# Optimization experiments

Hardware: AMD Instinct MI355X
Metric: run time of the kernel (lower is better)

The kernel has to match this reference:

```python
import jax, jax.numpy as jnp
import numpy as np

TS = 4  # tile_size


def _disp_upsample_slanted(d, dx, dy, ts):
    """Slanted-plane disparity upsample (PixelShuffle of per-tile-pixel planes).
    d, dx, dy: [B,1,Ht,Wt] -> full-res disparity [B,1,H,W], H=Ht*ts, W=Wt*ts.
    output[y,x] = d[y//ts,x//ts] + (y%ts - c)*dy + (x%ts - c)*dx, c=(ts-1)/2."""
    B, _, Ht, Wt = d.shape
    c = (ts - 1) / 2
    off = jnp.arange(ts, dtype=d.dtype) - jnp.asarray(c, d.dtype)  # [ts]
    d_, dx_, dy_ = d[:, 0], dx[:, 0], dy[:, 0]  # [B,Ht,Wt]
    off_i = off[None, :, None, None, None]  # row offset within tile
    off_j = off[None, None, :, None, None]  # col offset within tile
    disp = d_[:, None, None] + off_i * dy_[:, None, None] + off_j * dx_[:, None, None]
    # [B,ts_i,ts_j,Ht,Wt] -> pixel-shuffle -> [B,1,H,W]
    disp = disp.transpose(0, 3, 1, 4, 2).reshape(B, 1, Ht * ts, Wt * ts)
    return disp


def _l1_cost_chaos(fea_l, fea_r, disp):
    """Per-pixel horizontal warp of fea_r by continuous disparity (linear interp,
    zero outside image), then L1 distance over channels. Returns [B,1,H,W]."""
    B, C, H, W = fea_l.shape
    x = jnp.arange(W, dtype=disp.dtype)
    x_src = x[None, None, None, :] - disp              # [B,1,H,W]
    x0 = jnp.floor(x_src)
    w = (x_src - x0).astype(fea_r.dtype)
    x0i = jnp.clip(x0.astype(jnp.int32), 0, W - 1)
    x1i = jnp.clip(x0i + 1, 0, W - 1)
    f0 = jnp.take_along_axis(fea_r, jnp.broadcast_to(x0i, (B, C, H, W)), axis=3)
    f1 = jnp.take_along_axis(fea_r, jnp.broadcast_to(x1i, (B, C, H, W)), axis=3)
    warped = f0 * (1.0 - w) + f1 * w
    valid = (x_src >= 0) & (x_src <= W - 1)
    warped = jnp.where(valid, warped, jnp.zeros((), fea_r.dtype))
    return jnp.sum(jnp.abs(fea_l - warped), axis=1, keepdims=True)


def _tile_unshuffle(cv, ts):
    """[B,1,H,W] -> [B, ts*ts, H//ts, W//ts]; channel i*ts+j holds cv[i::ts, j::ts]."""
    B, _, H, W = cv.shape
    Ht, Wt = H // ts, W // ts
    return cv.reshape(B, Ht, ts, Wt, ts).transpose(0, 2, 4, 1, 3).reshape(B, ts * ts, Ht, Wt)


def setup_inputs() -> dict:
    key = jax.random.key(0)
    k1, k2, k3, k4, k5 = jax.random.split(key, 5)
    B, C, H, W, ts = 4, 32, 512, 960, TS
    Ht, Wt = H // ts, W // ts
    d = jax.random.uniform(k1, (B, 1, Ht, Wt), jnp.float32) * 48.0
    dx = jax.random.normal(k2, (B, 1, Ht, Wt), jnp.float32) * 0.1
    dy = jax.random.normal(k3, (B, 1, Ht, Wt), jnp.float32) * 0.1
    tile_plane = jnp.concatenate([d, dx, dy], axis=1)  # [B,3,Ht,Wt]
    fea_l = jax.random.normal(k4, (B, C, H, W), jnp.float32)
    fea_r = jax.random.normal(k5, (B, C, H, W), jnp.float32)
    return {"tile_plane": tile_plane, "fea_l": fea_l, "fea_r": fea_r}


def reference(tile_plane, fea_l, fea_r):
    ts = TS
    tile_d = tile_plane[:, 0:1]
    tile_dx = tile_plane[:, 1:2]
    tile_dy = tile_plane[:, 2:3]
    local_cv = []
    for disp_d in (-1, 0, 1):
        disp_full = _disp_upsample_slanted(tile_d + disp_d, tile_dx, tile_dy, ts)
        cv = _l1_cost_chaos(fea_l, fea_r, disp_full)        # [B,1,H,W]
        local_cv.append(_tile_unshuffle(cv, ts))            # [B,ts*ts,Ht,Wt]
    return jnp.concatenate(local_cv, axis=1)                # [B,3*ts*ts,Ht,Wt]
```

## Files before the change

kernel.cpp:

```cpp
#include <hip/hip_runtime.h>
#include <cstdint>

#define AS1 __attribute__((address_space(1)))
#define AS3 __attribute__((address_space(3)))

constexpr int B  = 4;
constexpr int C  = 32;
constexpr int H  = 512;
constexpr int Wd = 960;
constexpr int Ht = H / 4;
constexpr int Wt = Wd / 4;
constexpr int HW = H * Wd;

constexpr int BLKX  = 256;
constexpr int XMARG = 56;
constexpr int SELEM = BLKX + 64;

__global__ __launch_bounds__(256, 4) void tile_warping_kernel(
    const float* __restrict__ tp,
    const float* __restrict__ fl,
    const float* __restrict__ fr,
    float* __restrict__ out)
{
    __shared__ float sm[SELEM * C];

    const int lane = threadIdx.x;
    const int x0 = blockIdx.x * BLKX;
    const int y  = blockIdx.y;
    const int b  = blockIdx.z;
    const int xstart = x0 - XMARG;

    const float* frrow = fr + ((size_t)b * C * H + y) * Wd;
    #pragma unroll
    for (int chunk = 0; chunk < (SELEM * C) / (BLKX * 4); ++chunk) {
        int e   = chunk * (BLKX * 4) + lane * 4;
        int ch  = e / SELEM;
        int off = e - ch * SELEM;
        int gx  = min(max(xstart + off, 0), Wd - 4);
        const float* gp = frrow + (size_t)ch * HW + gx;
        __builtin_amdgcn_global_load_lds((const AS1 float*)gp,
                                         (AS3 float*)(&sm[e]), 16, 0, 0);
    }
    __syncthreads();

    const int x = x0 + lane;
    if (x < Wd) {
        const int ht = y >> 2, ii = y & 3;
        const int wt = x >> 2, jj = x & 3;

        const int tbase = ((b * 3) * Ht + ht) * Wt + wt;
        const float dv  = tp[tbase];
        const float dxv = tp[tbase + Ht * Wt];
        const float dyv = tp[tbase + 2 * Ht * Wt];

        const float oi = (float)ii - 1.5f;
        const float oj = (float)jj - 1.5f;

        int   o0[3];
        float w[3], w1[3];
        bool  val[3];
        #pragma unroll
        for (int k = 0; k < 3; ++k) {
            float disp = ((dv + (float)(k - 1)) + oi * dyv) + oj * dxv;
            float xs = (float)x - disp;
            float ff = floorf(xs);
            w[k]  = xs - ff;
            w1[k] = 1.0f - w[k];
            int c0 = min(max((int)ff, 0), Wd - 1);
            o0[k]  = c0 - xstart;
            val[k] = (xs >= 0.0f) && (xs <= (float)(Wd - 1));
        }

        const float* flp = fl + ((size_t)b * C * H + y) * Wd + x;

        float s0 = 0.f, s1 = 0.f, s2 = 0.f;
        #pragma unroll 4
        for (int c = 0; c < C; ++c) {
            float l = flp[(size_t)c * HW];
            const float* bp = sm + c * SELEM;
            float f00 = bp[o0[0]], f01 = bp[o0[0] + 1];
            float f10 = bp[o0[1]], f11 = bp[o0[1] + 1];
            float f20 = bp[o0[2]], f21 = bp[o0[2] + 1];
            float wv0 = val[0] ? (f00 * w1[0] + f01 * w[0]) : 0.f;
            float wv1 = val[1] ? (f10 * w1[1] + f11 * w[1]) : 0.f;
            float wv2 = val[2] ? (f20 * w1[2] + f21 * w[2]) : 0.f;
            s0 += fabsf(l - wv0);
            s1 += fabsf(l - wv1);
            s2 += fabsf(l - wv2);
        }

        const int obase = ((b * 48) * Ht + ht) * Wt + wt;
        out[obase + (0 * 16 + ii * 4 + jj) * (Ht * Wt)] = s0;
        out[obase + (1 * 16 + ii * 4 + jj) * (Ht * Wt)] = s1;
        out[obase + (2 * 16 + ii * 4 + jj) * (Ht * Wt)] = s2;
    }
}

extern "C" void kernel_launch(void* const* d_in, const int* in_sizes, int n_in,
                              void* d_out, int out_size, void* d_ws, size_t ws_size,
                              hipStream_t stream) {
    const float* tp = (const float*)d_in[0];
    const float* fl = (const float*)d_in[1];
    const float* fr = (const float*)d_in[2];
    float* out = (float*)d_out;

    dim3 grid((Wd + BLKX - 1) / BLKX, H, B);
    tile_warping_kernel<<<grid, 256, 0, stream>>>(tp, fl, fr, out);
}
```

Baseline: 492.7 us.

## Split channel staging into two LDS phases and share taps across disparity offsets

The right-feature row is now staged in LDS 16 channels at a time over two phases instead of all 32 at once. This halves shared memory per block so occupancy can rise, and launch bounds go from 4 to 8 blocks per CU. It also uses the fact that the three disparity hypotheses differ by exactly one pixel, so one floor and one weight pair are shared and only four consecutive LDS taps are read per channel instead of six. The cost is an extra pair of barriers and a second global-to-LDS load round per block, and the edge clamping that was done per hypothesis is replaced by fixed validity ranges.

Result: no change. 497.7 us (+1.0%).

```diff
diff --git a/kernel.cpp b/kernel.cpp
--- a/kernel.cpp
+++ b/kernel.cpp
@@ -15,14 +15,15 @@
 constexpr int BLKX  = 256;
 constexpr int XMARG = 56;
 constexpr int SELEM = BLKX + 64;
+constexpr int CH2   = 16;
 
-__global__ __launch_bounds__(256, 4) void tile_warping_kernel(
+__global__ __launch_bounds__(256, 8) void tile_warping_kernel(
     const float* __restrict__ tp,
     const float* __restrict__ fl,
     const float* __restrict__ fr,
     float* __restrict__ out)
 {
-    __shared__ float sm[SELEM * C];
+    __shared__ float sm[SELEM * CH2];
 
     const int lane = threadIdx.x;
     const int x0 = blockIdx.x * BLKX;
@@ -30,65 +31,73 @@
     const int b  = blockIdx.z;
     const int xstart = x0 - XMARG;
 
-    const float* frrow = fr + ((size_t)b * C * H + y) * Wd;
-    #pragma unroll
-    for (int chunk = 0; chunk < (SELEM * C) / (BLKX * 4); ++chunk) {
-        int e   = chunk * (BLKX * 4) + lane * 4;
-        int ch  = e / SELEM;
-        int off = e - ch * SELEM;
-        int gx  = min(max(xstart + off, 0), Wd - 4);
-        const float* gp = frrow + (size_t)ch * HW + gx;
-        __builtin_amdgcn_global_load_lds((const AS1 float*)gp,
-                                         (AS3 float*)(&sm[e]), 16, 0, 0);
-    }
-    __syncthreads();
+    const int x = x0 + lane;
+    const bool active = (x < Wd);
 
-    const int x = x0 + lane;
-    if (x < Wd) {
+    float w = 0.f, w1 = 0.f;
+    int om1 = 0;
+    bool val0 = false, val1 = false, val2 = false;
+    if (active) {
         const int ht = y >> 2, ii = y & 3;
         const int wt = x >> 2, jj = x & 3;
-
         const int tbase = ((b * 3) * Ht + ht) * Wt + wt;
         const float dv  = tp[tbase];
         const float dxv = tp[tbase + Ht * Wt];
         const float dyv = tp[tbase + 2 * Ht * Wt];
-
         const float oi = (float)ii - 1.5f;
         const float oj = (float)jj - 1.5f;
+        float disp = ((dv + 0.0f) + oi * dyv) + oj * dxv;
+        float xs = (float)x - disp;
+        float ff = floorf(xs);
+        w  = xs - ff;
+        w1 = 1.0f - w;
+        int F = (int)ff;
+        om1 = F - 1 - xstart;
+        val0 = (xs >= -1.0f) && (xs <= 958.0f);
+        val1 = (xs >=  0.0f) && (xs <= 959.0f);
+        val2 = (xs >=  1.0f) && (xs <= 960.0f);
+    }
 
-        int   o0[3];
-        float w[3], w1[3];
-        bool  val[3];
+    float s0 = 0.f, s1 = 0.f, s2 = 0.f;
+
+    for (int phase = 0; phase < 2; ++phase) {
+        const float* frrow = fr + (((size_t)b * C + phase * CH2) * H + y) * Wd;
         #pragma unroll
-        for (int k = 0; k < 3; ++k) {
-            float disp = ((dv + (float)(k - 1)) + oi * dyv) + oj * dxv;
-            float xs = (float)x - disp;
-            float ff = floorf(xs);
-            w[k]  = xs - ff;
-            w1[k] = 1.0f - w[k];
-            int c0 = min(max((int)ff, 0), Wd - 1);
-            o0[k]  = c0 - xstart;
-            val[k] = (xs >= 0.0f) && (xs <= (float)(Wd - 1));
+        for (int chunk = 0; chunk < (SELEM * CH2) / (BLKX * 4); ++chunk) {
+            int e   = chunk * (BLKX * 4) + lane * 4;
+            int ch  = e / SELEM;
+            int off = e - ch * SELEM;
+            int gx  = min(max(xstart + off, 0), Wd - 4);
+            const float* gp = frrow + (size_t)ch * HW + gx;
+            __builtin_amdgcn_global_load_lds((const AS1 float*)gp,
+                                             (AS3 float*)(&sm[e]), 16, 0, 0);
         }
+        __syncthreads();
 
-        const float* flp = fl + ((size_t)b * C * H + y) * Wd + x;
+        if (active) {
+            const float* flp = fl + (((size_t)b * C + phase * CH2) * H + y) * Wd + x;
+            #pragma unroll 4
+            for (int cc = 0; cc < CH2; ++cc) {
+                float l = flp[(size_t)cc * HW];
+                const float* bp = sm + cc * SELEM + om1;
+                float t0 = bp[0];
+                float t1 = bp[1];
+                float t2 = bp[2];
+                float t3 = bp[3];
+                float wv0 = val0 ? (t2 * w1 + t3 * w) : 0.f;
+                float wv1 = val1 ? (t1 * w1 + t2 * w) : 0.f;
+                float wv2 = val2 ? (t0 * w1 + t1 * w) : 0.f;
+                s0 += fabsf(l - wv0);
+                s1 += fabsf(l - wv1);
+                s2 += fabsf(l - wv2);
+            }
+        }
+        __syncthreads();
+    }
 
-        float s0 = 0.f, s1 = 0.f, s2 = 0.f;
-        #pragma unroll 4
-        for (int c = 0; c < C; ++c) {
-            float l = flp[(size_t)c * HW];
-            const float* bp = sm + c * SELEM;
-            float f00 = bp[o0[0]], f01 = bp[o0[0] + 1];
-            float f10 = bp[o0[1]], f11 = bp[o0[1] + 1];
-            float f20 = bp[o0[2]], f21 = bp[o0[2] + 1];
-            float wv0 = val[0] ? (f00 * w1[0] + f01 * w[0]) : 0.f;
-            float wv1 = val[1] ? (f10 * w1[1] + f11 * w[1]) : 0.f;
-            float wv2 = val[2] ? (f20 * w1[2] + f21 * w[2]) : 0.f;
-            s0 += fabsf(l - wv0);
-            s1 += fabsf(l - wv1);
-            s2 += fabsf(l - wv2);
-        }
-
+    if (active) {
+        const int ht = y >> 2, ii = y & 3;
+        const int wt = x >> 2, jj = x & 3;
         const int obase = ((b * 48) * Ht + ht) * Wt + wt;
         out[obase + (0 * 16 + ii * 4 + jj) * (Ht * Wt)] = s0;
         out[obase + (1 * 16 + ii * 4 + jj) * (Ht * Wt)] = s1;
```

## Prefetch left features into registers and share taps across the three disparity offsets

Applied to the files above, without the earlier changes.

All 32 channels of the left feature are loaded into registers before the LDS barrier, so global latency overlaps with the async right-feature LDS fill. The three disparity hypotheses differ by exactly one pixel, so they share one fractional weight and four consecutive LDS taps. This replaces six loads per channel with four and recomputes the floor and weights once instead of three times. It costs about 32 extra VGPRs, and clamping was removed in favour of validity masks, so edge behaviour relies on the zero masks being correct.

After: 681.9 us. 38.4% more time.

```diff
diff --git a/kernel.cpp b/kernel.cpp
--- a/kernel.cpp
+++ b/kernel.cpp
@@ -30,6 +30,10 @@
     const int b  = blockIdx.z;
     const int xstart = x0 - XMARG;
 
+    const int x = x0 + lane;
+    const bool active = (x < Wd);
+    const int xc = min(x, Wd - 1);
+
     const float* frrow = fr + ((size_t)b * C * H + y) * Wd;
     #pragma unroll
     for (int chunk = 0; chunk < (SELEM * C) / (BLKX * 4); ++chunk) {
@@ -41,54 +45,50 @@
         __builtin_amdgcn_global_load_lds((const AS1 float*)gp,
                                          (AS3 float*)(&sm[e]), 16, 0, 0);
     }
+
+    const float* flp = fl + ((size_t)b * C * H + y) * Wd + xc;
+    float lv[C];
+    #pragma unroll
+    for (int c = 0; c < C; ++c) lv[c] = flp[(size_t)c * HW];
+
+    const int ht = y >> 2, ii = y & 3;
+    const int wt = xc >> 2, jj = xc & 3;
+    const int tbase = ((b * 3) * Ht + ht) * Wt + wt;
+    const float dv  = tp[tbase];
+    const float dxv = tp[tbase + Ht * Wt];
+    const float dyv = tp[tbase + 2 * Ht * Wt];
+    const float oi = (float)ii - 1.5f;
+    const float oj = (float)jj - 1.5f;
+    float disp = ((dv + 0.0f) + oi * dyv) + oj * dxv;
+    float xs = (float)xc - disp;
+    float ff = floorf(xs);
+    const float w  = xs - ff;
+    const float w1 = 1.0f - w;
+    const int   om1 = (int)ff - 1 - xstart;
+    const bool val0 = (xs >= -1.0f) && (xs <= 958.0f);
+    const bool val1 = (xs >=  0.0f) && (xs <= 959.0f);
+    const bool val2 = (xs >=  1.0f) && (xs <= 960.0f);
+
     __syncthreads();
 
-    const int x = x0 + lane;
-    if (x < Wd) {
-        const int ht = y >> 2, ii = y & 3;
-        const int wt = x >> 2, jj = x & 3;
+    float s0 = 0.f, s1 = 0.f, s2 = 0.f;
+    #pragma unroll
+    for (int c = 0; c < C; ++c) {
+        float l = lv[c];
+        const float* bp = sm + c * SELEM + om1;
+        float t0 = bp[0];
+        float t1 = bp[1];
+        float t2 = bp[2];
+        float t3 = bp[3];
+        float wv0 = val0 ? (t2 * w1 + t3 * w) : 0.f;
+        float wv1 = val1 ? (t1 * w1 + t2 * w) : 0.f;
+        float wv2 = val2 ? (t0 * w1 + t1 * w) : 0.f;
+        s0 += fabsf(l - wv0);
+        s1 += fabsf(l - wv1);
+        s2 += fabsf(l - wv2);
+    }
 
-        const int tbase = ((b * 3) * Ht + ht) * Wt + wt;
-        const float dv  = tp[tbase];
-        const float dxv = tp[tbase + Ht * Wt];
-        const float dyv = tp[tbase + 2 * Ht * Wt];
-
-        const float oi = (float)ii - 1.5f;
-        const float oj = (float)jj - 1.5f;
-
-        int   o0[3];
-        float w[3], w1[3];
-        bool  val[3];
-        #pragma unroll
-        for (int k = 0; k < 3; ++k) {
-            float disp = ((dv + (float)(k - 1)) + oi * dyv) + oj * dxv;
-            float xs = (float)x - disp;
-            float ff = floorf(xs);
-            w[k]  = xs - ff;
-            w1[k] = 1.0f - w[k];
-            int c0 = min(max((int)ff, 0), Wd - 1);
-            o0[k]  = c0 - xstart;
-            val[k] = (xs >= 0.0f) && (xs <= (float)(Wd - 1));
-        }
-
-        const float* flp = fl + ((size_t)b * C * H + y) * Wd + x;
-
-        float s0 = 0.f, s1 = 0.f, s2 = 0.f;
-        #pragma unroll 4
-        for (int c = 0; c < C; ++c) {
-            float l = flp[(size_t)c * HW];
-            const float* bp = sm + c * SELEM;
-            float f00 = bp[o0[0]], f01 = bp[o0[0] + 1];
-            float f10 = bp[o0[1]], f11 = bp[o0[1] + 1];
-            float f20 = bp[o0[2]], f21 = bp[o0[2] + 1];
-            float wv0 = val[0] ? (f00 * w1[0] + f01 * w[0]) : 0.f;
-            float wv1 = val[1] ? (f10 * w1[1] + f11 * w[1]) : 0.f;
-            float wv2 = val[2] ? (f20 * w1[2] + f21 * w[2]) : 0.f;
-            s0 += fabsf(l - wv0);
-            s1 += fabsf(l - wv1);
-            s2 += fabsf(l - wv2);
-        }
-
+    if (active) {
         const int obase = ((b * 48) * Ht + ht) * Wt + wt;
         out[obase + (0 * 16 + ii * 4 + jj) * (Ht * Wt)] = s0;
         out[obase + (1 * 16 + ii * 4 + jj) * (Ht * Wt)] = s1;
```
